# Optimization experiments

Measured on AMD Instinct MI355X. Metric: run time of the kernel, lower is better.

The kernel has to match this reference:

```python
import jax, jax.numpy as jnp
import numpy as np

HEADS = 8

def conv1x1(x, w, b=None):
    # x: [b,c,h,w], w: [o,c]
    y = jnp.einsum('bchw,oc->bohw', x, w)
    if b is not None:
        y = y + b[None, :, None, None]
    return y

def dwconv3(x, w):
    # depthwise 3x3, SAME padding; w: [C,1,3,3]
    return jax.lax.conv_general_dilated(
        x, w, window_strides=(1, 1), padding='SAME',
        feature_group_count=x.shape[1],
        dimension_numbers=('NCHW', 'OIHW', 'NCHW'))

def layernorm_c(x, w, b):
    # WithBias LayerNorm over channel dim (torch normalizes last dim of b,(hw),c)
    mu = x.mean(axis=1, keepdims=True)
    var = ((x - mu) ** 2).mean(axis=1, keepdims=True)
    return (x - mu) / jnp.sqrt(var + 1e-5) * w[None, :, None, None] + b[None, :, None, None]

def l2norm_lastdim(x):
    n = jnp.sqrt(jnp.sum(x * x, axis=-1, keepdims=True))
    return x / jnp.maximum(n, 1e-12)

def channel_attention(xq, xkv, q_w, q_dw_w, kv_w, kv_dw_w, temperature, attn4, proj_w):
    b, c, h, w = xq.shape
    q = dwconv3(conv1x1(xq, q_w), q_dw_w)
    kv = dwconv3(conv1x1(xkv, kv_w), kv_dw_w)
    k, v = jnp.split(kv, 2, axis=1)
    ch = c // HEADS  # channels per head
    def heads(t):
        return t.reshape(b, HEADS, ch, h * w)
    q, k, v = heads(q), heads(k), heads(v)
    q = l2norm_lastdim(q)
    k = l2norm_lastdim(k)
    attn = jnp.einsum('bhcn,bhdn->bhcd', q, k) * temperature[None]  # [b,H,ch,ch]
    kk = int(ch * 0.9)
    thr = jax.lax.top_k(attn, kk)[0][..., -1:]
    masked = jnp.where(attn >= thr, attn, -jnp.inf)
    score = jax.nn.softmax(masked, axis=-1)
    out = jnp.einsum('bhcd,bhdn->bhcn', score, v) * attn4
    out = out.reshape(b, c, h, w)
    return conv1x1(out, proj_w)

def geglu_ffn(x, ffn_in_w, ffn_dw_w, ffn_out_w):
    y = conv1x1(x, ffn_in_w)
    y = dwconv3(y, ffn_dw_w)
    y1, y2 = jnp.split(y, 2, axis=1)
    return conv1x1(jax.nn.gelu(y1, approximate=False) * y2, ffn_out_w)


def reference(vi_featur, ir_featur, text_code,
              se_w1, se_w2, conv1x1_w, conv1x1_b, conv_out_w, conv_out_b,
              text_w1, text_b1, text_w2, text_b2,
              norm1_w, norm1_b, norm2_w, norm2_b, norm3_w, norm3_b,
              q_w, q_dw_w, kv_w, kv_dw_w, temperature, attn4, proj_w,
              ffn_in_w, ffn_dw_w, ffn_out_w):
    b, c, h, w = vi_featur.shape
    concat = jnp.concatenate([vi_featur, ir_featur], axis=1)  # [b,2c,h,w]
    squeeze = concat.mean(axis=(2, 3))                         # [b,2c]
    cw = jax.nn.sigmoid(jax.nn.relu(squeeze @ se_w1.T) @ se_w2.T)
    topk = c  # int(2*ch_dim*0.5)
    idx = jax.lax.top_k(cw, topk)[1]                           # [b,topk]
    selected = jnp.take_along_axis(concat, idx[:, :, None, None], axis=1)
    img = conv1x1(selected, conv1x1_w, conv1x1_b)              # [b,2c,h,w]
    tf = jax.nn.relu(text_code @ text_w1.T + text_b1) @ text_w2.T + text_b2  # [b,2c]
    soft_idx = jax.lax.top_k(tf, 2 * c)[1]                     # full descending perm
    shuffled = jnp.take_along_axis(img, soft_idx[:, :, None, None], axis=1)
    q_in = conv1x1(shuffled, conv_out_w, conv_out_b)           # [b,c,h,w]
    img_feature2 = conv1x1(concat, conv_out_w, conv_out_b)
    att = channel_attention(layernorm_c(q_in, norm1_w, norm1_b),
                            layernorm_c(img_feature2, norm2_w, norm2_b),
                            q_w, q_dw_w, kv_w, kv_dw_w, temperature, attn4, proj_w)
    output = att + geglu_ffn(layernorm_c(att, norm3_w, norm3_b), ffn_in_w, ffn_dw_w, ffn_out_w)
    return (output, img_feature2)


def setup_inputs() -> dict:
    key = jax.random.key(0)
    ks = jax.random.split(key, 20)
    B, C, H, W = 4, 128, 128, 128
    s = 0.05
    d = {
        'vi_featur': jax.random.normal(ks[0], (B, C, H, W), jnp.float32),
        'ir_featur': jax.random.normal(ks[1], (B, C, H, W), jnp.float32),
        'text_code': jax.random.normal(ks[2], (B, 512), jnp.float32),
        'se_w1': jax.random.normal(ks[3], (32, 256), jnp.float32) * s,
        'se_w2': jax.random.normal(ks[4], (256, 32), jnp.float32) * s,
        'conv1x1_w': jax.random.normal(ks[5], (256, 128), jnp.float32) * s,
        'conv1x1_b': jnp.zeros((256,), jnp.float32),
        'conv_out_w': jax.random.normal(ks[6], (128, 256), jnp.float32) * s,
        'conv_out_b': jnp.zeros((128,), jnp.float32),
        'text_w1': jax.random.normal(ks[7], (512, 512), jnp.float32) * s,
        'text_b1': jnp.zeros((512,), jnp.float32),
        'text_w2': jax.random.normal(ks[8], (256, 512), jnp.float32) * s,
        'text_b2': jnp.zeros((256,), jnp.float32),
        'norm1_w': jnp.ones((128,), jnp.float32), 'norm1_b': jnp.zeros((128,), jnp.float32),
        'norm2_w': jnp.ones((128,), jnp.float32), 'norm2_b': jnp.zeros((128,), jnp.float32),
        'norm3_w': jnp.ones((128,), jnp.float32), 'norm3_b': jnp.zeros((128,), jnp.float32),
        'q_w': jax.random.normal(ks[9], (128, 128), jnp.float32) * s,
        'q_dw_w': jax.random.normal(ks[10], (128, 1, 3, 3), jnp.float32) * s,
        'kv_w': jax.random.normal(ks[11], (256, 128), jnp.float32) * s,
        'kv_dw_w': jax.random.normal(ks[12], (256, 1, 3, 3), jnp.float32) * s,
        'temperature': jnp.ones((8, 1, 1), jnp.float32),
        'attn4': jnp.ones((1,), jnp.float32) * 0.2,
        'proj_w': jax.random.normal(ks[13], (128, 128), jnp.float32) * s,
        'ffn_in_w': jax.random.normal(ks[14], (680, 128), jnp.float32) * s,
        'ffn_dw_w': jax.random.normal(ks[15], (680, 1, 3, 3), jnp.float32) * s,
        'ffn_out_w': jax.random.normal(ks[16], (128, 340), jnp.float32) * s,
    }
    return d
```

## Files before the change

kernel.cpp:

```cpp
#include <hip/hip_runtime.h>

typedef unsigned short u16;
typedef __attribute__((ext_vector_type(8))) short bf16x8;
typedef __attribute__((ext_vector_type(4))) float f32x4;

#define N_PIX 16384
static constexpr long NP = 4L * 128 * N_PIX;

__device__ __forceinline__ float bf2f(u16 h) {
  unsigned u = ((unsigned)h) << 16; float f; __builtin_memcpy(&f, &u, 4); return f;
}
__device__ __forceinline__ u16 f2bf(float f) {
  unsigned u; __builtin_memcpy(&u, &f, 4);
  u = (u + 0x7fffu + ((u >> 16) & 1u)) >> 16; return (u16)u;
}

__device__ __forceinline__ float blockReduceSum256(float v) {
  #pragma unroll
  for (int o = 32; o > 0; o >>= 1) v += __shfl_down(v, o, 64);
  __shared__ float sw[4];
  int lane = threadIdx.x & 63, w = threadIdx.x >> 6;
  if (lane == 0) sw[w] = v;
  __syncthreads();
  return (threadIdx.x == 0) ? (sw[0] + sw[1] + sw[2] + sw[3]) : 0.f;
}

__global__ __launch_bounds__(256) void wconv3_k(const float* __restrict__ a0, u16* __restrict__ o0, long n0,
                                                const float* __restrict__ a1, u16* __restrict__ o1, long n1,
                                                const float* __restrict__ a2, u16* __restrict__ o2, long n2) {
  long i = (long)blockIdx.x * 256 + threadIdx.x;
  if (i < n0) o0[i] = f2bf(a0[i]);
  if (i < n1) o1[i] = f2bf(a1[i]);
  if (i < n2) o2[i] = f2bf(a2[i]);
}

__global__ __launch_bounds__(256) void squeeze_k(const float* __restrict__ vi,
                                                 const float* __restrict__ ir,
                                                 float* __restrict__ sq,
                                                 u16* __restrict__ cbf) {
  int c = blockIdx.x, b = blockIdx.y, tid = threadIdx.x;
  const float* src = (c < 128) ? (vi + ((long)b * 128 + c) * N_PIX)
                               : (ir + ((long)b * 128 + (c - 128)) * N_PIX);
  const f32x4* src4 = (const f32x4*)src;
  u16* dst = cbf + ((long)b * 256 + c) * N_PIX;
  float s = 0.f;
  #pragma unroll
  for (int j = 0; j < 8; ++j) {
    f32x4 v0 = src4[j * 512 + tid * 2];
    f32x4 v1 = src4[j * 512 + tid * 2 + 1];
    s += v0.x + v0.y + v0.z + v0.w + v1.x + v1.y + v1.z + v1.w;
    bf16x8 r;
    r[0] = (short)f2bf(v0.x); r[1] = (short)f2bf(v0.y);
    r[2] = (short)f2bf(v0.z); r[3] = (short)f2bf(v0.w);
    r[4] = (short)f2bf(v1.x); r[5] = (short)f2bf(v1.y);
    r[6] = (short)f2bf(v1.z); r[7] = (short)f2bf(v1.w);
    *(bf16x8*)(dst + j * 2048 + tid * 8) = r;
  }
  float t = blockReduceSum256(s);
  if (tid == 0) sq[b * 256 + c] = t * (1.f / 16384.f);
}

__global__ __launch_bounds__(256) void se_text1_k(const float* __restrict__ sq,
                                                  const float* __restrict__ sew1,
                                                  const float* __restrict__ sew2,
                                                  int* __restrict__ idx,
                                                  const float* __restrict__ tc,
                                                  const float* __restrict__ tw1,
                                                  const float* __restrict__ tb1,
                                                  float* __restrict__ t1f) {
  int b = blockIdx.y, tid = threadIdx.x;
  __shared__ float sm[544];
  if (blockIdx.x == 64) {
    float* s_sq = sm; float* s_h1 = sm + 256; float* s_cw = sm + 288;
    s_sq[tid] = sq[b * 256 + tid];
    __syncthreads();
    if (tid < 32) {
      float s = 0.f;
      for (int c = 0; c < 256; ++c) s += s_sq[c] * sew1[tid * 256 + c];
      s_h1[tid] = fmaxf(s, 0.f);
    }
    __syncthreads();
    {
      float s = 0.f;
      #pragma unroll
      for (int j = 0; j < 32; ++j) s += s_h1[j] * sew2[tid * 32 + j];
      s_cw[tid] = 1.f / (1.f + expf(-s));
    }
    __syncthreads();
    float my = s_cw[tid];
    int rk = 0;
    for (int c = 0; c < 256; ++c) {
      float o = s_cw[c];
      rk += (o > my) || (o == my && c < tid);
    }
    if (rk < 128) idx[b * 128 + rk] = tid;
  } else {
    float* s_tc = sm;
    int j0 = blockIdx.x * 8;
    s_tc[tid] = tc[b * 512 + tid];
    s_tc[tid + 256] = tc[b * 512 + 256 + tid];
    __syncthreads();
    int w = tid >> 6, lane = tid & 63;
    #pragma unroll
    for (int r = 0; r < 2; ++r) {
      int j = j0 + w * 2 + r;
      const float* wr = tw1 + (long)j * 512;
      float s = 0.f;
      #pragma unroll
      for (int k = 0; k < 8; ++k) s += s_tc[lane + k * 64] * wr[lane + k * 64];
      #pragma unroll
      for (int o = 32; o > 0; o >>= 1) s += __shfl_down(s, o, 64);
      if (lane == 0) t1f[b * 512 + j] = fmaxf(s + tb1[j], 0.f);
    }
  }
}

__global__ __launch_bounds__(256) void text2_k(const float* __restrict__ t1f,
                                               const float* __restrict__ tw2,
                                               const float* __restrict__ tb2,
                                               float* __restrict__ tf) {
  int b = blockIdx.y, j0 = blockIdx.x * 8, tid = threadIdx.x;
  __shared__ float s_t1[512];
  s_t1[tid] = t1f[b * 512 + tid];
  s_t1[tid + 256] = t1f[b * 512 + 256 + tid];
  __syncthreads();
  int w = tid >> 6, lane = tid & 63;
  #pragma unroll
  for (int r = 0; r < 2; ++r) {
    int j = j0 + w * 2 + r;
    const float* wr = tw2 + (long)j * 512;
    float s = 0.f;
    #pragma unroll
    for (int k = 0; k < 8; ++k) s += s_t1[lane + k * 64] * wr[lane + k * 64];
    #pragma unroll
    for (int o = 32; o > 0; o >>= 1) s += __shfl_down(s, o, 64);
    if (lane == 0) tf[b * 256 + j] = s + tb2[j];
  }
}

__global__ __launch_bounds__(256) void rank2_k(const float* __restrict__ tf,
                                               int* __restrict__ sidx) {
  int b = blockIdx.x, tid = threadIdx.x;
  __shared__ float s_tf[256];
  s_tf[tid] = tf[b * 256 + tid];
  __syncthreads();
  float my = s_tf[tid];
  int rk = 0;
  for (int c = 0; c < 256; ++c) {
    float o = s_tf[c];
    rk += (o > my) || (o == my && c < tid);
  }
  sidx[b * 256 + rk] = tid;
}

__global__ __launch_bounds__(128) void mcomb_k(const float* __restrict__ w2,
                                               const float* __restrict__ w2b,
                                               const float* __restrict__ w1,
                                               const float* __restrict__ w1b,
                                               const int* __restrict__ idx,
                                               const int* __restrict__ sidx,
                                               u16* __restrict__ mch,
                                               u16* __restrict__ mcl,
                                               float* __restrict__ bcomb) {
  int o = blockIdx.x, b = blockIdx.y, tid = threadIdx.x;
  __shared__ float s_w2[256];
  __shared__ int s_sx[256];
  s_w2[tid] = w2[o * 256 + tid];
  s_w2[tid + 128] = w2[o * 256 + tid + 128];
  s_sx[tid] = sidx[b * 256 + tid] & 255;
  s_sx[tid + 128] = sidx[b * 256 + tid + 128] & 255;
  u16* hrow = mch + ((long)b * 128 + o) * 256;
  u16* lrow = mcl + ((long)b * 128 + o) * 256;
  hrow[tid] = 0; hrow[tid + 128] = 0;
  lrow[tid] = 0; lrow[tid + 128] = 0;
  __syncthreads();
  float s = 0.f;
  for (int j = 0; j < 256; ++j) s += s_w2[j] * w1[s_sx[j] * 128 + tid];
  int cc = idx[b * 128 + tid] & 255;
  u16 hi = f2bf(s);
  hrow[cc] = hi;
  lrow[cc] = f2bf(s - bf2f(hi));
  if (tid == 0) {
    float bb = w2b[o];
    for (int j = 0; j < 256; ++j) bb += s_w2[j] * w1b[s_sx[j]];
    bcomb[b * 128 + o] = bb;
  }
}

__global__ __launch_bounds__(256) void gemm_dual_k(
    const u16* __restrict__ W2b, const float* __restrict__ b2,
    const u16* __restrict__ Mch, const u16* __restrict__ Mcl,
    const float* __restrict__ bc, const u16* __restrict__ Xb,
    float* __restrict__ out1, u16* __restrict__ qin) {
  const int N = N_PIX;
  int n0 = blockIdx.x * 64, o0 = blockIdx.y * 64, bz = blockIdx.z, tid = threadIdx.x;
  __shared__ __align__(16) u16 A1[64][72];
  __shared__ __align__(16) u16 A2h[64][72];
  __shared__ __align__(16) u16 A2l[64][72];
  __shared__ __align__(16) u16 Xs[64][72];
  f32x4 acc1[4], acc2[4];
  #pragma unroll
  for (int i = 0; i < 4; ++i) { acc1[i] = (f32x4){0,0,0,0}; acc2[i] = (f32x4){0,0,0,0}; }
  int wv = tid >> 6, lane = tid & 63;
  int lr = lane & 15, lkq = (lane >> 4) * 8;
  for (int kt = 0; kt < 4; ++kt) {
    int k0 = kt << 6;
    {
      int r = tid >> 2, o = o0 + r;
      #pragma unroll
      for (int cc = 0; cc < 2; ++cc) {
        int col = ((tid & 3) << 3) + cc * 32;
        int k = k0 + col;
        *(bf16x8*)&A1[r][col] = *(const bf16x8*)(W2b + (long)o * 256 + k);
        *(bf16x8*)&A2h[r][col] = *(const bf16x8*)(Mch + ((long)bz * 128 + o) * 256 + k);
        *(bf16x8*)&A2l[r][col] = *(const bf16x8*)(Mcl + ((long)bz * 128 + o) * 256 + k);
      }
    }
    {
      int n = tid & 63;
      const u16* src = Xb + (long)bz * 256 * N + n0 + n;
      #pragma unroll
      for (int cc = 0; cc < 2; ++cc) {
        int kb = ((tid >> 6) << 3) + cc * 32;
        int k = k0 + kb;
        bf16x8 t;
        #pragma unroll
        for (int i = 0; i < 8; ++i) t[i] = (short)src[(long)(k + i) * N];
        *(bf16x8*)&Xs[n][kb] = t;
      }
    }
    __syncthreads();
    #pragma unroll
    for (int kk = 0; kk < 2; ++kk) {
      int lk = kk * 32 + lkq;
      bf16x8 a1 = *(const bf16x8*)&A1[wv * 16 + lr][lk];
      bf16x8 a2h = *(const bf16x8*)&A2h[wv * 16 + lr][lk];
      bf16x8 a2l = *(const bf16x8*)&A2l[wv * 16 + lr][lk];
      #pragma unroll
      for (int nt = 0; nt < 4; ++nt) {
        bf16x8 bfr = *(const bf16x8*)&Xs[nt * 16 + lr][lk];
        acc1[nt] = __builtin_amdgcn_mfma_f32_16x16x32_bf16(a1, bfr, acc1[nt], 0, 0, 0);
        acc2[nt] = __builtin_amdgcn_mfma_f32_16x16x32_bf16(a2h, bfr, acc2[nt], 0, 0, 0);
        acc2[nt] = __builtin_amdgcn_mfma_f32_16x16x32_bf16(a2l, bfr, acc2[nt], 0, 0, 0);
      }
    }
    if (kt < 3) __syncthreads();
  }
  #pragma unroll
  for (int nt = 0; nt < 4; ++nt)
    #pragma unroll
    for (int r4 = 0; r4 < 4; ++r4) {
      int o = o0 + wv * 16 + (lane >> 4) * 4 + r4;
      int n = n0 + nt * 16 + (lane & 15);
      long oi = ((long)bz * 128 + o) * N + n;
      out1[oi] = acc1[nt][r4] + b2[o];
      qin[oi] = f2bf(acc2[nt][r4] + bc[bz * 128 + o]);
    }
}

__device__ __forceinline__ bf16x8 ldA_f32(const float* ap) {
  f32x4 v0 = *(const f32x4*)ap, v1 = *(const f32x4*)(ap + 4);
  bf16x8 w8;
  w8[0] = (short)f2bf(v0.x); w8[1] = (short)f2bf(v0.y);
  w8[2] = (short)f2bf(v0.z); w8[3] = (short)f2bf(v0.w);
  w8[4] = (short)f2bf(v1.x); w8[5] = (short)f2bf(v1.y);
  w8[6] = (short)f2bf(v1.z); w8[7] = (short)f2bf(v1.w);
  return w8;
}

template<int AMODE, int RESADD, int OUTF>
__global__ __launch_bounds__(256) void gemm_k(
    const float* __restrict__ Af, const u16* __restrict__ Ah,
    const u16* __restrict__ Alo, long a_bstride,
    const u16* __restrict__ X, long x_bstride,
    const u16* __restrict__ res, long res_bstride,
    void* __restrict__ outv, long out_bstride,
    int O, int K) {
  const int N = N_PIX;
  int n0 = blockIdx.x * 64;
  int o0 = blockIdx.y * 64;
  int bz = blockIdx.z;
  int tid = threadIdx.x;
  __shared__ __align__(16) u16 As[64][136];
  __shared__ __align__(16) u16 Al[(AMODE == 3) ? 64 : 1][136];
  __shared__ __align__(16) u16 Xs[64][136];
  f32x4 acc[4];
  #pragma unroll
  for (int i = 0; i < 4; ++i) acc[i] = (f32x4){0.f, 0.f, 0.f, 0.f};
  int wv = tid >> 6, lane = tid & 63;
  int lr = lane & 15, lkq = (lane >> 4) * 8;
  int nk = (K + 127) >> 7;
  for (int kt = 0; kt < nk; ++kt) {
    int k0 = kt << 7;
    {
      int r = tid >> 2, o = o0 + r;
      #pragma unroll
      for (int cc = 0; cc < 4; ++cc) {
        int col = ((tid & 3) << 3) + cc * 32;
        int k = k0 + col;
        if (AMODE == 0) {
          bf16x8 w8;
          if (o < O && k + 8 <= K) {
            w8 = ldA_f32(Af + (long)o * K + k);
          } else {
            #pragma unroll
            for (int i = 0; i < 8; ++i)
              w8[i] = (short)((o < O && k + i < K) ? f2bf(Af[(long)o * K + k + i]) : (u16)0);
          }
          *(bf16x8*)&As[r][col] = w8;
        } else if (AMODE == 2) {
          bf16x8 t;
          if (o < O && k + 8 <= K) {
            t = *(const bf16x8*)(Ah + (long)o * K + k);
          } else {
            #pragma unroll
            for (int i = 0; i < 8; ++i)
              t[i] = (short)((o < O && k + i < K) ? Ah[(long)o * K + k + i] : (u16)0);
          }
          *(bf16x8*)&As[r][col] = t;
        } else {
          long base = (long)bz * a_bstride + (long)o * K + k;
          *(bf16x8*)&As[r][col] = *(const bf16x8*)(Ah + base);
          *(bf16x8*)&Al[r][col] = *(const bf16x8*)(Alo + base);
        }
      }
    }
    {
      int n = tid & 63;
      const u16* src = X + (long)bz * x_bstride + n0 + n;
      #pragma unroll
      for (int cc = 0; cc < 4; ++cc) {
        int kb = ((tid >> 6) << 3) + cc * 32;
        int k = k0 + kb;
        bf16x8 t;
        #pragma unroll
        for (int i = 0; i < 8; ++i)
          t[i] = (short)((k + i < K) ? src[(long)(k + i) * N] : (u16)0);
        *(bf16x8*)&Xs[n][kb] = t;
      }
    }
    __syncthreads();
    #pragma unroll
    for (int kk = 0; kk < 4; ++kk) {
      int lk = kk * 32 + lkq;
      bf16x8 afr = *(const bf16x8*)&As[wv * 16 + lr][lk];
      bf16x8 alr;
      if (AMODE == 3) alr = *(const bf16x8*)&Al[wv * 16 + lr][lk];
      #pragma unroll
      for (int nt = 0; nt < 4; ++nt) {
        bf16x8 bfr = *(const bf16x8*)&Xs[nt * 16 + lr][lk];
        acc[nt] = __builtin_amdgcn_mfma_f32_16x16x32_bf16(afr, bfr, acc[nt], 0, 0, 0);
        if (AMODE == 3)
          acc[nt] = __builtin_amdgcn_mfma_f32_16x16x32_bf16(alr, bfr, acc[nt], 0, 0, 0);
      }
    }
    if (kt + 1 < nk) __syncthreads();
  }
  #pragma unroll
  for (int nt = 0; nt < 4; ++nt)
    #pragma unroll
    for (int r4 = 0; r4 < 4; ++r4) {
      int o = o0 + wv * 16 + (lane >> 4) * 4 + r4;
      int n = n0 + nt * 16 + (lane & 15);
      if (o < O) {
        float v = acc[nt][r4];
        if (RESADD) v += bf2f(res[(long)bz * res_bstride + (long)o * N + n]);
        long oi = (long)bz * out_bstride + (long)o * N + n;
        if (OUTF) ((float*)outv)[oi] = v;
        else ((u16*)outv)[oi] = f2bf(v);
      }
    }
}

__global__ __launch_bounds__(256) void ln12_k(const u16* __restrict__ qin,
                                              const float* __restrict__ o1,
                                              const float* __restrict__ g1,
                                              const float* __restrict__ b1,
                                              const float* __restrict__ g2,
                                              const float* __restrict__ b2,
                                              u16* __restrict__ xq,
                                              u16* __restrict__ xkv) {
  int p0 = blockIdx.x * 64, y = blockIdx.y, tid = threadIdx.x;
  bool second = (y >= 4);
  int b = second ? y - 4 : y;
  const float* gamma = second ? g2 : g1;
  const float* beta  = second ? b2 : b1;
  u16* out = second ? xkv : xq;
  int px = tid & 63, g4 = tid >> 6;
  __shared__ float tile[128][65];
  __shared__ float red[8][64];
  __shared__ float gmm[128], bta[128], mu_s[64], rs_s[64];
  if (tid < 128) { gmm[tid] = gamma[tid]; bta[tid] = beta[tid]; }
  long bofs = (long)b * 128 * N_PIX;
  float s = 0.f;
  for (int c = g4; c < 128; c += 4) {
    long ix = bofs + (long)c * N_PIX + p0 + px;
    float v = second ? o1[ix] : bf2f(qin[ix]);
    tile[c][px] = v;
    s += v;
  }
  red[g4][px] = s;
  __syncthreads();
  if (g4 == 0) mu_s[px] = (red[0][px] + red[1][px] + red[2][px] + red[3][px]) * (1.f / 128.f);
  __syncthreads();
  float mu = mu_s[px];
  float s2 = 0.f;
  for (int c = g4; c < 128; c += 4) { float d = tile[c][px] - mu; s2 += d * d; }
  red[4 + g4][px] = s2;
  __syncthreads();
  if (g4 == 0) {
    float var = (red[4][px] + red[5][px] + red[6][px] + red[7][px]) * (1.f / 128.f);
    rs_s[px] = rsqrtf(var + 1e-5f);
  }
  __syncthreads();
  float rs = rs_s[px];
  for (int c = g4; c < 128; c += 4)
    out[bofs + (long)c * N_PIX + p0 + px] = f2bf((tile[c][px] - mu) * rs * gmm[c] + bta[c]);
}

__global__ __launch_bounds__(256) void ln_k(const u16* __restrict__ in,
                                            const float* __restrict__ gamma,
                                            const float* __restrict__ beta,
                                            u16* __restrict__ out) {
  int p0 = blockIdx.x * 64, b = blockIdx.y, tid = threadIdx.x;
  int px = tid & 63, g4 = tid >> 6;
  __shared__ float tile[128][65];
  __shared__ float red[8][64];
  __shared__ float gmm[128], bta[128], mu_s[64], rs_s[64];
  if (tid < 128) { gmm[tid] = gamma[tid]; bta[tid] = beta[tid]; }
  long bofs = (long)b * 128 * N_PIX;
  float s = 0.f;
  for (int c = g4; c < 128; c += 4) {
    float v = bf2f(in[bofs + (long)c * N_PIX + p0 + px]);
    tile[c][px] = v;
    s += v;
  }
  red[g4][px] = s;
  __syncthreads();
  if (g4 == 0) mu_s[px] = (red[0][px] + red[1][px] + red[2][px] + red[3][px]) * (1.f / 128.f);
  __syncthreads();
  float mu = mu_s[px];
  float s2 = 0.f;
  for (int c = g4; c < 128; c += 4) { float d = tile[c][px] - mu; s2 += d * d; }
  red[4 + g4][px] = s2;
  __syncthreads();
  if (g4 == 0) {
    float var = (red[4][px] + red[5][px] + red[6][px] + red[7][px]) * (1.f / 128.f);
    rs_s[px] = rsqrtf(var + 1e-5f);
  }
  __syncthreads();
  float rs = rs_s[px];
  for (int c = g4; c < 128; c += 4)
    out[bofs + (long)c * N_PIX + p0 + px] = f2bf((tile[c][px] - mu) * rs * gmm[c] + bta[c]);
}

__global__ __launch_bounds__(256) void dw3t2_k(const u16* __restrict__ inQ,
                                               const float* __restrict__ wQ,
                                               u16* __restrict__ outQ,
                                               const u16* __restrict__ inKV,
                                               const float* __restrict__ wKV,
                                               u16* __restrict__ outKV) {
  int gp = blockIdx.x >> 3, stripe = blockIdx.x & 7, tid = threadIdx.x;
  const u16* in; const float* w; u16* out; int c; long pbase;
  if (gp < 512) { in = inQ;  w = wQ;  out = outQ;  c = gp & 127;  pbase = (long)gp * N_PIX; }
  else { int p2 = gp - 512; in = inKV; w = wKV; out = outKV; c = p2 & 255; pbase = (long)p2 * N_PIX; }
  int y0 = stripe * 16;
  __shared__ __align__(16) u16 tile[18][136];
  for (int v = tid; v < 288; v += 256) {
    int r = v >> 4, col = (v & 15) << 3;
    int y = y0 - 1 + r;
    bf16x8 t;
    #pragma unroll
    for (int i = 0; i < 8; ++i) t[i] = 0;
    if (y >= 0 && y < 128) t = *(const bf16x8*)(in + pbase + y * 128 + col);
    *(bf16x8*)&tile[r][col] = t;
  }
  float wv[9];
  #pragma unroll
  for (int j = 0; j < 9; ++j) wv[j] = w[c * 9 + j];
  __syncthreads();
  int row = tid >> 4, col0 = (tid & 15) << 3;
  float a[3][10];
  #pragma unroll
  for (int dr = 0; dr < 3; ++dr)
    #pragma unroll
    for (int i = 0; i < 10; ++i) {
      int x = col0 - 1 + i;
      a[dr][i] = (x >= 0 && x < 128) ? bf2f(tile[row + dr][x]) : 0.f;
    }
  bf16x8 res;
  #pragma unroll
  for (int j = 0; j < 8; ++j) {
    float s = 0.f;
    #pragma unroll
    for (int dr = 0; dr < 3; ++dr)
      #pragma unroll
      for (int dx = 0; dx < 3; ++dx) s += wv[dr * 3 + dx] * a[dr][j + dx];
    res[j] = (short)f2bf(s);
  }
  *(bf16x8*)(out + pbase + (y0 + row) * 128 + col0) = res;
}

__global__ __launch_bounds__(256) void dw3gelu4_k(const u16* __restrict__ ft,
                                                  const float* __restrict__ w,
                                                  u16* __restrict__ fg) {
  int plane = blockIdx.x >> 3, stripe = blockIdx.x & 7, tid = threadIdx.x;
  int b = plane / 340, c = plane % 340;
  const u16* t1 = ft + ((long)b * 680 + c) * N_PIX;
  const u16* t2 = ft + ((long)b * 680 + 340 + c) * N_PIX;
  u16* g = fg + ((long)b * 340 + c) * N_PIX;
  int y0 = stripe * 16;
  __shared__ __align__(16) u16 ta[18][136];
  __shared__ __align__(16) u16 tb[18][136];
  for (int v = tid; v < 288; v += 256) {
    int r = v >> 4, col = (v & 15) << 3;
    int y = y0 - 1 + r;
    bf16x8 u1, u2;
    #pragma unroll
    for (int i = 0; i < 8; ++i) { u1[i] = 0; u2[i] = 0; }
    if (y >= 0 && y < 128) {
      u1 = *(const bf16x8*)(t1 + y * 128 + col);
      u2 = *(const bf16x8*)(t2 + y * 128 + col);
    }
    *(bf16x8*)&ta[r][col] = u1;
    *(bf16x8*)&tb[r][col] = u2;
  }
  float w1[9], w2[9];
  #pragma unroll
  for (int j = 0; j < 9; ++j) { w1[j] = w[c * 9 + j]; w2[j] = w[(340 + c) * 9 + j]; }
  __syncthreads();
  int row = tid >> 4, col0 = (tid & 15) << 3;
  float a[3][10], bb[3][10];
  #pragma unroll
  for (int dr = 0; dr < 3; ++dr)
    #pragma unroll
    for (int i = 0; i < 10; ++i) {
      int x = col0 - 1 + i;
      bool ok = (x >= 0 && x < 128);
      a[dr][i] = ok ? bf2f(ta[row + dr][x]) : 0.f;
      bb[dr][i] = ok ? bf2f(tb[row + dr][x]) : 0.f;
    }
  bf16x8 res;
  #pragma unroll
  for (int j = 0; j < 8; ++j) {
    float s1 = 0.f, s2 = 0.f;
    #pragma unroll
    for (int dr = 0; dr < 3; ++dr)
      #pragma unroll
      for (int dx = 0; dx < 3; ++dx) {
        s1 += w1[dr * 3 + dx] * a[dr][j + dx];
        s2 += w2[dr * 3 + dx] * bb[dr][j + dx];
      }
    float gl = 0.5f * s1 * (1.f + erff(s1 * 0.70710678118f));
    res[j] = (short)f2bf(gl * s2);
  }
  *(bf16x8*)(g + (y0 + row) * 128 + col0) = res;
}

__global__ __launch_bounds__(256) void rownorm2_k(const u16* __restrict__ q,
                                                  const u16* __restrict__ kv,
                                                  float* __restrict__ qn,
                                                  float* __restrict__ kn) {
  int x = blockIdx.x, b = blockIdx.y, tid = threadIdx.x;
  const u16* src;
  float* dst;
  if (x < 128) { src = q + (long)b * 128 * N_PIX + (long)x * N_PIX; dst = qn + b * 128 + x; }
  else { int r = x - 128; src = kv + (long)b * 256 * N_PIX + (long)r * N_PIX; dst = kn + b * 128 + r; }
  float s = 0.f;
  #pragma unroll
  for (int j = 0; j < 8; ++j) {
    bf16x8 v = *(const bf16x8*)(src + j * 2048 + tid * 8);
    #pragma unroll
    for (int i = 0; i < 8; ++i) { float f = bf2f((u16)v[i]); s += f * f; }
  }
  float t = blockReduceSum256(s);
  if (tid == 0) *dst = sqrtf(t);
}

__global__ __launch_bounds__(256) void attn_part_k(const u16* __restrict__ q,
                                                   const u16* __restrict__ kbase,
                                                   long kbstride,
                                                   float* __restrict__ part) {
  int ch = blockIdx.x, h = blockIdx.y, b = blockIdx.z, tid = threadIdx.x;
  int n0 = ch * 256;
  __shared__ __align__(16) u16 qc[16][280];
  __shared__ __align__(16) u16 kc[16][280];
  #pragma unroll
  for (int j = 0; j < 2; ++j) {
    int v = tid + j * 256;
    int r = v >> 5, col = (v & 31) << 3;
    *(bf16x8*)&qc[r][col] = *(const bf16x8*)(q + ((long)b * 128 + h * 16 + r) * N_PIX + n0 + col);
    *(bf16x8*)&kc[r][col] = *(const bf16x8*)(kbase + (long)b * kbstride + (long)(h * 16 + r) * N_PIX + n0 + col);
  }
  __syncthreads();
  int c = tid >> 4, d = tid & 15;
  float acc = 0.f;
  #pragma unroll 4
  for (int nb = 0; nb < 32; ++nb) {
    bf16x8 qv = *(const bf16x8*)&qc[c][nb * 8];
    bf16x8 kv = *(const bf16x8*)&kc[d][nb * 8];
    #pragma unroll
    for (int i = 0; i < 8; ++i) acc += bf2f((u16)qv[i]) * bf2f((u16)kv[i]);
  }
  part[(long)((((b * 8 + h) * 16 + c) * 16 + d)) * 64 + ch] = acc;
}

__global__ __launch_bounds__(256) void attn_reduce_k(const float* __restrict__ part,
                                                     const float* __restrict__ qn,
                                                     const float* __restrict__ kn,
                                                     const float* __restrict__ temp,
                                                     float* __restrict__ attnm) {
  int idx = blockIdx.x * 256 + threadIdx.x;
  const float* p = part + (long)idx * 64;
  float s = 0.f;
  #pragma unroll
  for (int j = 0; j < 64; ++j) s += p[j];
  int d = idx & 15, c = (idx >> 4) & 15, h = (idx >> 8) & 7, b = idx >> 11;
  float nq = fmaxf(qn[b * 128 + h * 16 + c], 1e-12f);
  float nk = fmaxf(kn[b * 128 + h * 16 + d], 1e-12f);
  attnm[idx] = s / (nq * nk) * temp[h];
}

__global__ __launch_bounds__(128) void score_cmb_k(const float* __restrict__ attnm,
                                                   const float* __restrict__ projw,
                                                   const float* __restrict__ attn4p,
                                                   u16* __restrict__ cmbh,
                                                   u16* __restrict__ cmbl) {
  int b = blockIdx.x, tid = threadIdx.x;
  __shared__ float att_s[2048], score_s[2048];
  for (int i = tid; i < 2048; i += 128) att_s[i] = attnm[(long)b * 2048 + i];
  __syncthreads();
  {
    int h = tid >> 4, c = tid & 15;
    float v[16], t[16];
    #pragma unroll
    for (int d = 0; d < 16; ++d) { v[d] = att_s[(h * 16 + c) * 16 + d]; t[d] = v[d]; }
    float thr = 0.f, M = -1e30f;
    for (int it = 0; it < 14; ++it) {
      float m = -1e30f; int mi = 0;
      #pragma unroll
      for (int d = 0; d < 16; ++d) if (t[d] > m) { m = t[d]; mi = d; }
      if (it == 0) M = m;
      thr = m;
      t[mi] = -1e31f;
    }
    float s = 0.f, e[16];
    #pragma unroll
    for (int d = 0; d < 16; ++d) { e[d] = (v[d] >= thr) ? expf(v[d] - M) : 0.f; s += e[d]; }
    float inv = 1.f / s;
    #pragma unroll
    for (int d = 0; d < 16; ++d) score_s[(h * 16 + c) * 16 + d] = e[d] * inv;
  }
  __syncthreads();
  float a4 = attn4p[0];
  int o = tid;
  for (int hd = 0; hd < 128; ++hd) {
    int h = hd >> 4, d = hd & 15;
    float s = 0.f;
    #pragma unroll
    for (int c = 0; c < 16; ++c)
      s += projw[o * 128 + h * 16 + c] * score_s[(h * 16 + c) * 16 + d];
    float v = a4 * s;
    long oi = ((long)b * 128 + o) * 128 + hd;
    u16 hi = f2bf(v);
    cmbh[oi] = hi;
    cmbl[oi] = f2bf(v - bf2f(hi));
  }
}

extern "C" void kernel_launch(void* const* d_in, const int* in_sizes, int n_in,
                              void* d_out, int out_size, void* d_ws, size_t ws_size,
                              hipStream_t stream) {
  (void)in_sizes; (void)n_in; (void)out_size; (void)ws_size;
  const float* vi        = (const float*)d_in[0];
  const float* ir        = (const float*)d_in[1];
  const float* text_code = (const float*)d_in[2];
  const float* se_w1     = (const float*)d_in[3];
  const float* se_w2     = (const float*)d_in[4];
  const float* conv1x1_w = (const float*)d_in[5];
  const float* conv1x1_b = (const float*)d_in[6];
  const float* conv_out_w= (const float*)d_in[7];
  const float* conv_out_b= (const float*)d_in[8];
  const float* text_w1   = (const float*)d_in[9];
  const float* text_b1   = (const float*)d_in[10];
  const float* text_w2   = (const float*)d_in[11];
  const float* text_b2   = (const float*)d_in[12];
  const float* norm1_w   = (const float*)d_in[13];
  const float* norm1_b   = (const float*)d_in[14];
  const float* norm2_w   = (const float*)d_in[15];
  const float* norm2_b   = (const float*)d_in[16];
  const float* norm3_w   = (const float*)d_in[17];
  const float* norm3_b   = (const float*)d_in[18];
  const float* q_w       = (const float*)d_in[19];
  const float* q_dw_w    = (const float*)d_in[20];
  const float* kv_w      = (const float*)d_in[21];
  const float* kv_dw_w   = (const float*)d_in[22];
  const float* temperature = (const float*)d_in[23];
  const float* attn4     = (const float*)d_in[24];
  const float* proj_w    = (const float*)d_in[25];
  const float* ffn_in_w  = (const float*)d_in[26];
  const float* ffn_dw_w  = (const float*)d_in[27];
  const float* ffn_out_w = (const float*)d_in[28];
  float* out0 = (float*)d_out;
  float* out1 = out0 + NP;

  char* W = (char*)d_ws;
  float* sq_f  = (float*)(W + 0);
  int*   idx_i = (int*)(W + 4096);
  int*   sidx_i= (int*)(W + 6144);
  u16*   Mch   = (u16*)(W + 12288);
  u16*   Mcl   = (u16*)(W + 274432);
  float* bcomb = (float*)(W + 536576);
  float* qn_f  = (float*)(W + 538624);
  float* kn_f  = (float*)(W + 540672);
  float* attnm = (float*)(W + 542720);
  u16*   cmbh  = (u16*)(W + 575488);
  u16*   cmbl  = (u16*)(W + 706560);
  float* t1f   = (float*)(W + 834560);
  float* tf_f  = (float*)(W + 842752);
  u16*   W2b   = (u16*)(W + 846848);
  u16*   qwb   = (u16*)(W + 912384);
  u16*   kvwb  = (u16*)(W + 945152);
  u16* S   = (u16*)(W + (1 << 20));
  u16* CC  = S;
  u16* KD  = S + 512L * N_PIX;
  u16* CBF = S + 1024L * N_PIX;
  u16* QT  = S + 1024L * N_PIX;
  u16* KVD = S + 1024L * N_PIX;
  u16* FT4 = S + 2048L * N_PIX;
  u16* FG4 = S + 4768L * N_PIX;
  u16* KVT = (u16*)out0;
  u16* ATT = KD;

  const long SN = 128L * N_PIX;
  const long SN2 = 256L * N_PIX;

  wconv3_k<<<128, 256, 0, stream>>>(conv_out_w, W2b, 32768, q_w, qwb, 16384, kv_w, kvwb, 32768);
  squeeze_k<<<dim3(256, 4), 256, 0, stream>>>(vi, ir, sq_f, CBF);
  se_text1_k<<<dim3(65, 4), 256, 0, stream>>>(sq_f, se_w1, se_w2, idx_i,
                                              text_code, text_w1, text_b1, t1f);
  text2_k<<<dim3(32, 4), 256, 0, stream>>>(t1f, text_w2, text_b2, tf_f);
  rank2_k<<<4, 256, 0, stream>>>(tf_f, sidx_i);
  mcomb_k<<<dim3(128, 4), 128, 0, stream>>>(conv_out_w, conv_out_b, conv1x1_w,
                                            conv1x1_b, idx_i, sidx_i, Mch, Mcl, bcomb);
  gemm_dual_k<<<dim3(256, 2, 4), 256, 0, stream>>>(
      W2b, conv_out_b, Mch, Mcl, bcomb, CBF, out1, CC);
  ln12_k<<<dim3(256, 8), 256, 0, stream>>>(CC, out1, norm1_w, norm1_b,
                                           norm2_w, norm2_b, CC, KD);
  gemm_k<2, 0, 0><<<dim3(256, 2, 4), 256, 0, stream>>>(
      nullptr, qwb, nullptr, 0, CC, SN, nullptr, 0, QT, SN, 128, 128);
  gemm_k<2, 0, 0><<<dim3(256, 4, 4), 256, 0, stream>>>(
      nullptr, kvwb, nullptr, 0, KD, SN, nullptr, 0, KVT, SN2, 256, 128);
  dw3t2_k<<<12288, 256, 0, stream>>>(QT, q_dw_w, CC, KVT, kv_dw_w, KVD);
  rownorm2_k<<<dim3(256, 4), 256, 0, stream>>>(CC, KVD, qn_f, kn_f);
  float* part = (float*)out0;
  attn_part_k<<<dim3(64, 8, 4), 256, 0, stream>>>(CC, KVD, SN2, part);
  attn_reduce_k<<<32, 256, 0, stream>>>(part, qn_f, kn_f, temperature, attnm);
  score_cmb_k<<<4, 128, 0, stream>>>(attnm, proj_w, attn4, cmbh, cmbl);
  gemm_k<3, 0, 0><<<dim3(256, 2, 4), 256, 0, stream>>>(
      nullptr, cmbh, cmbl, 128L * 128, KVD + SN, SN2, nullptr, 0, ATT, SN, 128, 128);
  ln_k<<<dim3(256, 4), 256, 0, stream>>>(ATT, norm3_w, norm3_b, CC);
  gemm_k<0, 0, 0><<<dim3(256, 11, 4), 256, 0, stream>>>(
      ffn_in_w, nullptr, nullptr, 0, CC, SN, nullptr, 0, FT4, 680L * N_PIX, 680, 128);
  dw3gelu4_k<<<10880, 256, 0, stream>>>(FT4, ffn_dw_w, FG4);
  gemm_k<0, 1, 1><<<dim3(256, 2, 4), 256, 0, stream>>>(
      ffn_out_w, nullptr, nullptr, 0, FG4, 340L * N_PIX, ATT, SN,
      out0, SN, 128, 340);
}
```

Before: 419.6 us.

## Emit LayerNorm outputs pixel-major so K=128 GEMMs load X contiguously

The LayerNorm kernels now normalize into shared memory and write their bf16 output transposed ([pixel][channel]). A new XT mode in the GEMM reads that layout with 16-byte vector loads per row instead of strided scalar gathers across channels. The q/kv projections and the FFN-in GEMM use this path. Workspace buffers are remapped to hold the transposed tensors, which shifts the FFN buffers and adds an extra shared-memory pass in the LayerNorm kernels.

```diff
diff --git a/kernel.cpp b/kernel.cpp
--- a/kernel.cpp
+++ b/kernel.cpp
@@ -268,7 +268,7 @@
   return w8;
 }
 
-template<int AMODE, int RESADD, int OUTF>
+template<int AMODE, int RESADD, int OUTF, int XT>
 __global__ __launch_bounds__(256) void gemm_k(
     const float* __restrict__ Af, const u16* __restrict__ Ah,
     const u16* __restrict__ Alo, long a_bstride,
@@ -289,7 +289,7 @@
   for (int i = 0; i < 4; ++i) acc[i] = (f32x4){0.f, 0.f, 0.f, 0.f};
   int wv = tid >> 6, lane = tid & 63;
   int lr = lane & 15, lkq = (lane >> 4) * 8;
-  int nk = (K + 127) >> 7;
+  int nk = XT ? 1 : ((K + 127) >> 7);
   for (int kt = 0; kt < nk; ++kt) {
     int k0 = kt << 7;
     {
@@ -325,7 +325,13 @@
         }
       }
     }
-    {
+    if (XT) {
+      int n = tid >> 2, koff = (tid & 3) << 5;
+      const u16* src = X + (long)bz * x_bstride + (long)(n0 + n) * 128 + koff;
+      #pragma unroll
+      for (int j = 0; j < 4; ++j)
+        *(bf16x8*)&Xs[n][koff + j * 8] = *(const bf16x8*)(src + j * 8);
+    } else {
       int n = tid & 63;
       const u16* src = X + (long)bz * x_bstride + n0 + n;
       #pragma unroll
@@ -372,20 +378,20 @@
     }
 }
 
-__global__ __launch_bounds__(256) void ln12_k(const u16* __restrict__ qin,
-                                              const float* __restrict__ o1,
-                                              const float* __restrict__ g1,
-                                              const float* __restrict__ b1,
-                                              const float* __restrict__ g2,
-                                              const float* __restrict__ b2,
-                                              u16* __restrict__ xq,
-                                              u16* __restrict__ xkv) {
+__global__ __launch_bounds__(256) void ln12t_k(const u16* __restrict__ qin,
+                                               const float* __restrict__ o1,
+                                               const float* __restrict__ g1,
+                                               const float* __restrict__ b1,
+                                               const float* __restrict__ g2,
+                                               const float* __restrict__ b2,
+                                               u16* __restrict__ xqT,
+                                               u16* __restrict__ xkvT) {
   int p0 = blockIdx.x * 64, y = blockIdx.y, tid = threadIdx.x;
   bool second = (y >= 4);
   int b = second ? y - 4 : y;
   const float* gamma = second ? g2 : g1;
   const float* beta  = second ? b2 : b1;
-  u16* out = second ? xkv : xq;
+  u16* outT = second ? xkvT : xqT;
   int px = tid & 63, g4 = tid >> 6;
   __shared__ float tile[128][65];
   __shared__ float red[8][64];
@@ -415,13 +421,23 @@
   __syncthreads();
   float rs = rs_s[px];
   for (int c = g4; c < 128; c += 4)
-    out[bofs + (long)c * N_PIX + p0 + px] = f2bf((tile[c][px] - mu) * rs * gmm[c] + bta[c]);
-}
-
-__global__ __launch_bounds__(256) void ln_k(const u16* __restrict__ in,
-                                            const float* __restrict__ gamma,
-                                            const float* __restrict__ beta,
-                                            u16* __restrict__ out) {
+    tile[c][px] = (tile[c][px] - mu) * rs * gmm[c] + bta[c];
+  __syncthreads();
+  int px2 = tid >> 2, c0 = (tid & 3) << 5;
+  u16* dst = outT + ((long)b * N_PIX + p0 + px2) * 128 + c0;
+  #pragma unroll
+  for (int j = 0; j < 4; ++j) {
+    bf16x8 r;
+    #pragma unroll
+    for (int i = 0; i < 8; ++i) r[i] = (short)f2bf(tile[c0 + j * 8 + i][px2]);
+    *(bf16x8*)(dst + j * 8) = r;
+  }
+}
+
+__global__ __launch_bounds__(256) void lnt_k(const u16* __restrict__ in,
+                                             const float* __restrict__ gamma,
+                                             const float* __restrict__ beta,
+                                             u16* __restrict__ outT) {
   int p0 = blockIdx.x * 64, b = blockIdx.y, tid = threadIdx.x;
   int px = tid & 63, g4 = tid >> 6;
   __shared__ float tile[128][65];
@@ -451,7 +467,17 @@
   __syncthreads();
   float rs = rs_s[px];
   for (int c = g4; c < 128; c += 4)
-    out[bofs + (long)c * N_PIX + p0 + px] = f2bf((tile[c][px] - mu) * rs * gmm[c] + bta[c]);
+    tile[c][px] = (tile[c][px] - mu) * rs * gmm[c] + bta[c];
+  __syncthreads();
+  int px2 = tid >> 2, c0 = (tid & 3) << 5;
+  u16* dst = outT + ((long)b * N_PIX + p0 + px2) * 128 + c0;
+  #pragma unroll
+  for (int j = 0; j < 4; ++j) {
+    bf16x8 r;
+    #pragma unroll
+    for (int i = 0; i < 8; ++i) r[i] = (short)f2bf(tile[c0 + j * 8 + i][px2]);
+    *(bf16x8*)(dst + j * 8) = r;
+  }
 }
 
 __global__ __launch_bounds__(256) void dw3t2_k(const u16* __restrict__ inQ,
@@ -721,16 +747,18 @@
   u16*   W2b   = (u16*)(W + 846848);
   u16*   qwb   = (u16*)(W + 912384);
   u16*   kvwb  = (u16*)(W + 945152);
-  u16* S   = (u16*)(W + (1 << 20));
-  u16* CC  = S;
-  u16* KD  = S + 512L * N_PIX;
-  u16* CBF = S + 1024L * N_PIX;
-  u16* QT  = S + 1024L * N_PIX;
-  u16* KVD = S + 1024L * N_PIX;
-  u16* FT4 = S + 2048L * N_PIX;
-  u16* FG4 = S + 4768L * N_PIX;
-  u16* KVT = (u16*)out0;
-  u16* ATT = KD;
+  u16* S    = (u16*)(W + (1 << 20));
+  u16* CC   = S;
+  u16* KD   = S + 512L * N_PIX;
+  u16* CBF  = S + 1024L * N_PIX;
+  u16* KVD  = S + 1024L * N_PIX;
+  u16* XQT  = S + 2048L * N_PIX;
+  u16* X3T  = S + 2048L * N_PIX;
+  u16* XKVT = S + 2560L * N_PIX;
+  u16* FT4  = S + 2560L * N_PIX;
+  u16* FG4  = S + 5280L * N_PIX;
+  u16* KVT  = (u16*)out0;
+  u16* ATT  = KD;
 
   const long SN = 128L * N_PIX;
   const long SN2 = 256L * N_PIX;
@@ -745,25 +773,25 @@
                                             conv1x1_b, idx_i, sidx_i, Mch, Mcl, bcomb);
   gemm_dual_k<<<dim3(256, 2, 4), 256, 0, stream>>>(
       W2b, conv_out_b, Mch, Mcl, bcomb, CBF, out1, CC);
-  ln12_k<<<dim3(256, 8), 256, 0, stream>>>(CC, out1, norm1_w, norm1_b,
-                                           norm2_w, norm2_b, CC, KD);
-  gemm_k<2, 0, 0><<<dim3(256, 2, 4), 256, 0, stream>>>(
-      nullptr, qwb, nullptr, 0, CC, SN, nullptr, 0, QT, SN, 128, 128);
-  gemm_k<2, 0, 0><<<dim3(256, 4, 4), 256, 0, stream>>>(
-      nullptr, kvwb, nullptr, 0, KD, SN, nullptr, 0, KVT, SN2, 256, 128);
-  dw3t2_k<<<12288, 256, 0, stream>>>(QT, q_dw_w, CC, KVT, kv_dw_w, KVD);
+  ln12t_k<<<dim3(256, 8), 256, 0, stream>>>(CC, out1, norm1_w, norm1_b,
+                                            norm2_w, norm2_b, XQT, XKVT);
+  gemm_k<2, 0, 0, 1><<<dim3(256, 2, 4), 256, 0, stream>>>(
+      nullptr, qwb, nullptr, 0, XQT, SN, nullptr, 0, KD, SN, 128, 128);
+  gemm_k<2, 0, 0, 1><<<dim3(256, 4, 4), 256, 0, stream>>>(
+      nullptr, kvwb, nullptr, 0, XKVT, SN, nullptr, 0, KVT, SN2, 256, 128);
+  dw3t2_k<<<12288, 256, 0, stream>>>(KD, q_dw_w, CC, KVT, kv_dw_w, KVD);
   rownorm2_k<<<dim3(256, 4), 256, 0, stream>>>(CC, KVD, qn_f, kn_f);
   float* part = (float*)out0;
   attn_part_k<<<dim3(64, 8, 4), 256, 0, stream>>>(CC, KVD, SN2, part);
   attn_reduce_k<<<32, 256, 0, stream>>>(part, qn_f, kn_f, temperature, attnm);
   score_cmb_k<<<4, 128, 0, stream>>>(attnm, proj_w, attn4, cmbh, cmbl);
-  gemm_k<3, 0, 0><<<dim3(256, 2, 4), 256, 0, stream>>>(
+  gemm_k<3, 0, 0, 0><<<dim3(256, 2, 4), 256, 0, stream>>>(
       nullptr, cmbh, cmbl, 128L * 128, KVD + SN, SN2, nullptr, 0, ATT, SN, 128, 128);
-  ln_k<<<dim3(256, 4), 256, 0, stream>>>(ATT, norm3_w, norm3_b, CC);
-  gemm_k<0, 0, 0><<<dim3(256, 11, 4), 256, 0, stream>>>(
-      ffn_in_w, nullptr, nullptr, 0, CC, SN, nullptr, 0, FT4, 680L * N_PIX, 680, 128);
+  lnt_k<<<dim3(256, 4), 256, 0, stream>>>(ATT, norm3_w, norm3_b, X3T);
+  gemm_k<0, 0, 0, 1><<<dim3(256, 11, 4), 256, 0, stream>>>(
+      ffn_in_w, nullptr, nullptr, 0, X3T, SN, nullptr, 0, FT4, 680L * N_PIX, 680, 128);
   dw3gelu4_k<<<10880, 256, 0, stream>>>(FT4, ffn_dw_w, FG4);
-  gemm_k<0, 1, 1><<<dim3(256, 2, 4), 256, 0, stream>>>(
+  gemm_k<0, 1, 1, 0><<<dim3(256, 2, 4), 256, 0, stream>>>(
       ffn_out_w, nullptr, nullptr, 0, FG4, 340L * N_PIX, ATT, SN,
       out0, SN, 128, 340);
 }
```

Result: faster. 406.7 us (-3.1%).
